# Kernel optimization log

Hardware: AMD Instinct MI355X
Metric: run time of the kernel (lower is better)

Reference implementation:

```python
import jax, jax.numpy as jnp
import numpy as np

N, INC, MID, K = 65536, 256, 64, 16
EPS = 1e-5  # BatchNorm1d default eps


def _bn(x, g, b, m, v):
    # eval-mode BatchNorm1d applied per-channel along the last dim
    return (x - m) * (g * jax.lax.rsqrt(v + EPS)) + b


def setup_inputs() -> dict:
    key = jax.random.key(0)
    ks = jax.random.split(key, 40)
    rn = lambda i, shape, s=0.05: (jax.random.normal(ks[i], shape, jnp.float32) * s)
    pv = lambda i, n: jax.random.uniform(ks[i], (n,), jnp.float32, 0.5, 1.5)  # positive running var
    return {
        "feats": jax.random.normal(ks[0], (N, INC), jnp.float32),
        "pos": jax.random.uniform(ks[1], (N, 3), jnp.float32) * 10.0,
        "idx": jax.random.randint(ks[2], (N, K), 0, N),
        "w_in": rn(3, (MID, INC)),
        "w_q": rn(4, (MID, MID)), "b_q": rn(5, (MID,)),
        "w_k": rn(6, (MID, MID)), "b_k": rn(7, (MID,)),
        "w_v": rn(8, (MID, MID)), "b_v": rn(9, (MID,)),
        # pos_enc: Linear(3,3) -> BN(3) -> ReLU -> Linear(3,mid) -> BN(mid) -> ReLU
        "pe_w1": rn(10, (3, 3)), "pe_b1": rn(11, (3,)),
        "pe_g1": jnp.ones(3), "pe_be1": rn(12, (3,)), "pe_m1": rn(13, (3,)), "pe_v1": pv(14, 3),
        "pe_w2": rn(15, (MID, 3)), "pe_b2": rn(16, (MID,)),
        "pe_g2": jnp.ones(MID), "pe_be2": rn(17, (MID,)), "pe_m2": rn(18, (MID,)), "pe_v2": pv(19, MID),
        # mlp_gamma: Linear(mid,mid) -> BN(mid) -> ReLU -> Linear(mid,mid) -> BN(mid) -> ReLU
        "ga_w1": rn(20, (MID, MID)), "ga_b1": rn(21, (MID,)),
        "ga_g1": jnp.ones(MID), "ga_be1": rn(22, (MID,)), "ga_m1": rn(23, (MID,)), "ga_v1": pv(24, MID),
        "ga_w2": rn(25, (MID, MID)), "ga_b2": rn(26, (MID,)),
        "ga_g2": jnp.ones(MID), "ga_be2": rn(27, (MID,)), "ga_m2": rn(28, (MID,)), "ga_v2": pv(29, MID),
        "w_out": rn(30, (INC, MID)),
    }


def reference(feats, pos, w_in, w_q, b_q, w_k, b_k, w_v, b_v,
              pe_w1, pe_b1, pe_g1, pe_be1, pe_m1, pe_v1,
              pe_w2, pe_b2, pe_g2, pe_be2, pe_m2, pe_v2,
              ga_w1, ga_b1, ga_g1, ga_be1, ga_m1, ga_v1,
              ga_w2, ga_b2, ga_g2, ga_be2, ga_m2, ga_v2,
              w_out, idx):
    xx = feats @ w_in.T                              # [N, mid]
    q = xx @ w_q.T + b_q
    k = xx @ w_k.T + b_k
    v = xx @ w_v.T + b_v
    xv = v[idx]                                      # [N, K, mid] gather
    xk = k[idx]                                      # [N, K, mid]
    xpos = pos[idx]                                  # [N, K, 3]
    # pos_enc
    p = jax.nn.relu(_bn(xpos @ pe_w1.T + pe_b1, pe_g1, pe_be1, pe_m1, pe_v1))
    p = jax.nn.relu(_bn(p @ pe_w2.T + pe_b2, pe_g2, pe_be2, pe_m2, pe_v2))  # [N, K, mid]
    # vector attention logits
    w = xk - q[:, None, :] + p                       # [N, K, mid]
    # mlp_gamma
    w = jax.nn.relu(_bn(w @ ga_w1.T + ga_b1, ga_g1, ga_be1, ga_m1, ga_v1))
    w = jax.nn.relu(_bn(w @ ga_w2.T + ga_b2, ga_g2, ga_be2, ga_m2, ga_v2))
    w = jax.nn.softmax(w, axis=1)                    # softmax over neighbors
    out = jnp.sum((xv + p) * w, axis=1)              # [N, mid]
    out = out @ w_out.T                              # [N, inc]
    return out + feats
```

## Files before the change

kernel.cpp:

```cpp
#include <hip/hip_runtime.h>

#define NPTS 65536
#define INC  256
#define MID  64
#define KNB  16
#define WSTR 72

#define WIN_S   0
#define WQ_S    16384
#define WK_S    20480
#define WV_S    24576
#define GA1_S   28672
#define GA2_S   32768
#define WOUT_S  36864
#define NFRAG_ENT 6656

typedef __attribute__((ext_vector_type(8))) short short8;
typedef __attribute__((ext_vector_type(4))) float f32x4;

#define MFMA(a, b, c) __builtin_amdgcn_mfma_f32_16x16x32_bf16((a), (b), (c), 0, 0, 0)
#define WBAR() __builtin_amdgcn_wave_barrier()

__device__ inline float bf2f(unsigned short s) {
    unsigned int u = ((unsigned int)s) << 16;
    return __builtin_bit_cast(float, u);
}
__device__ inline unsigned int pk_bf16(float lo, float hi) {
    unsigned int r;
    asm("v_cvt_pk_bf16_f32 %0, %1, %2" : "=v"(r) : "v"(lo), "v"(hi));
    return r;
}
__device__ inline short f2bf(float f) { return (short)pk_bf16(f, f); }

__device__ inline short8 cvtf8(f32x4 a, f32x4 b) {
    union { unsigned int u[4]; short8 s; } r;
    r.u[0] = pk_bf16(a[0], a[1]); r.u[1] = pk_bf16(a[2], a[3]);
    r.u[2] = pk_bf16(b[0], b[1]); r.u[3] = pk_bf16(b[2], b[3]);
    return r.s;
}
__device__ inline short8 load_cvt8(const float* __restrict__ p) {
    const f32x4* v = (const f32x4*)p;
    return cvtf8(v[0], v[1]);
}
__device__ inline short8 load_cvt8s(const float* __restrict__ p, float scale) {
    const f32x4* v = (const f32x4*)p;
    f32x4 a = v[0], b = v[1];
    #pragma unroll
    for (int i = 0; i < 4; i++) { a[i] *= scale; b[i] *= scale; }
    return cvtf8(a, b);
}

__global__ __launch_bounds__(256) void k_prep(
    const float* __restrict__ w_in, const float* __restrict__ w_q,
    const float* __restrict__ w_k, const float* __restrict__ w_v,
    const float* __restrict__ ga_w1, const float* __restrict__ ga_w2,
    const float* __restrict__ w_out,
    const float* __restrict__ ga_g1, const float* __restrict__ ga_v1,
    const float* __restrict__ ga_g2, const float* __restrict__ ga_v2,
    short* __restrict__ wbuf)
{
    int gid = blockIdx.x * 256 + threadIdx.x;
    if (gid >= NFRAG_ENT) return;
    if (gid < 2048) {
        int e = gid, f = e >> 6, ln = e & 63;
        int nt = f & 3, ks = f >> 2;
        int row = nt * 16 + (ln & 15), col = ks * 32 + (ln >> 4) * 8;
        *(short8*)&wbuf[(size_t)gid * 8] = load_cvt8(w_in + (size_t)row * INC + col);
    } else if (gid < 4608) {
        int seg = (gid - 2048) >> 9;
        int e = (gid - 2048) & 511;
        const float* m = seg == 0 ? w_q : seg == 1 ? w_k : seg == 2 ? w_v
                       : seg == 3 ? ga_w1 : ga_w2;
        int f = e >> 6, ln = e & 63;
        int nt = f & 3, ks = f >> 2;
        int row = nt * 16 + (ln & 15), col = ks * 32 + (ln >> 4) * 8;
        float scale = 1.f;
        if (seg == 3)      scale = ga_g1[row] * rsqrtf(ga_v1[row] + 1e-5f);
        else if (seg == 4) scale = ga_g2[row] * rsqrtf(ga_v2[row] + 1e-5f);
        *(short8*)&wbuf[(size_t)gid * 8] = load_cvt8s(m + (size_t)row * MID + col, scale);
    } else {
        int e = gid - 4608, f = e >> 6, ln = e & 63;
        int nt = f >> 1, ks = f & 1;
        int row = nt * 16 + (ln & 15), col = ks * 32 + (ln >> 4) * 8;
        *(short8*)&wbuf[(size_t)gid * 8] = load_cvt8(w_out + (size_t)row * MID + col);
    }
}

__global__ __launch_bounds__(256) void k_qkv(
    const float* __restrict__ feats, const short* __restrict__ wfrag,
    const float* __restrict__ pos,
    const float* __restrict__ b_q, const float* __restrict__ b_k,
    const float* __restrict__ b_v,
    const float* __restrict__ pe_w1, const float* __restrict__ pe_b1,
    const float* __restrict__ pe_g1, const float* __restrict__ pe_be1,
    const float* __restrict__ pe_m1, const float* __restrict__ pe_v1,
    const float* __restrict__ pe_w2, const float* __restrict__ pe_b2,
    const float* __restrict__ pe_g2, const float* __restrict__ pe_be2,
    const float* __restrict__ pe_m2, const float* __restrict__ pe_v2,
    const float* __restrict__ ga_b1, const float* __restrict__ ga_g1,
    const float* __restrict__ ga_be1, const float* __restrict__ ga_m1,
    const float* __restrict__ ga_v1,
    short* __restrict__ q1f_out, short* __restrict__ k1_out,
    short* __restrict__ vp_out)
{
    __shared__ __align__(16) short XL[4][16 * WSTR];
    __shared__ float PS[4][16 * 4];
    const int tid = threadIdx.x;
    const int wave = tid >> 6, lane = tid & 63;
    const int l15 = lane & 15, quad = lane >> 4;
    const int rb = (blockIdx.x * 4 + wave) * 16;

    if (lane < 16) {
        float s0 = pe_g1[0] * rsqrtf(pe_v1[0] + 1e-5f);
        float s1 = pe_g1[1] * rsqrtf(pe_v1[1] + 1e-5f);
        float sc = pe_g1[2] * rsqrtf(pe_v1[2] + 1e-5f);
        float px = pos[(size_t)(rb + lane) * 3 + 0];
        float py = pos[(size_t)(rb + lane) * 3 + 1];
        float pz = pos[(size_t)(rb + lane) * 3 + 2];
        PS[wave][lane * 4 + 0] =
            fmaxf((px * pe_w1[0] + py * pe_w1[1] + pz * pe_w1[2] + pe_b1[0] - pe_m1[0]) * s0 + pe_be1[0], 0.f);
        PS[wave][lane * 4 + 1] =
            fmaxf((px * pe_w1[3] + py * pe_w1[4] + pz * pe_w1[5] + pe_b1[1] - pe_m1[1]) * s1 + pe_be1[1], 0.f);
        PS[wave][lane * 4 + 2] =
            fmaxf((px * pe_w1[6] + py * pe_w1[7] + pz * pe_w1[8] + pe_b1[2] - pe_m1[2]) * sc + pe_be1[2], 0.f);
    }

    float w2c0[4], w2c1[4], w2c2[4], s2c[4], sh2c[4], bet1[4], bqc[4], bkc[4], bvc[4];
    #pragma unroll
    for (int nt = 0; nt < 4; nt++) {
        int ch = nt * 16 + l15;
        w2c0[nt] = pe_w2[ch * 3 + 0]; w2c1[nt] = pe_w2[ch * 3 + 1]; w2c2[nt] = pe_w2[ch * 3 + 2];
        float s2 = pe_g2[ch] * rsqrtf(pe_v2[ch] + 1e-5f);
        s2c[nt] = s2;
        sh2c[nt] = (pe_b2[ch] - pe_m2[ch]) * s2 + pe_be2[ch];
        float s1 = ga_g1[ch] * rsqrtf(ga_v1[ch] + 1e-5f);
        bet1[nt] = ga_b1[ch] * s1 + ga_be1[ch] - ga_m1[ch] * s1;
        bqc[nt] = b_q[ch]; bkc[nt] = b_k[ch]; bvc[nt] = b_v[ch];
    }

    f32x4 acc[4];
    #pragma unroll
    for (int nt = 0; nt < 4; nt++) acc[nt] = (f32x4){0.f, 0.f, 0.f, 0.f};
    const float* arow = feats + (size_t)(rb + l15) * INC + quad * 8;
    #pragma unroll
    for (int ks = 0; ks < 8; ks++) {
        short8 a = load_cvt8(arow + ks * 32);
        #pragma unroll
        for (int nt = 0; nt < 4; nt++) {
            short8 b = *(const short8*)&wfrag[WIN_S + (size_t)((ks * 4 + nt) * 64 + lane) * 8];
            acc[nt] = MFMA(a, b, acc[nt]);
        }
    }
    #pragma unroll
    for (int nt = 0; nt < 4; nt++) {
        unsigned int p01 = pk_bf16(acc[nt][0], acc[nt][1]);
        unsigned int p23 = pk_bf16(acc[nt][2], acc[nt][3]);
        XL[wave][(quad * 4 + 0) * WSTR + nt * 16 + l15] = (short)p01;
        XL[wave][(quad * 4 + 1) * WSTR + nt * 16 + l15] = (short)(p01 >> 16);
        XL[wave][(quad * 4 + 2) * WSTR + nt * 16 + l15] = (short)p23;
        XL[wave][(quad * 4 + 3) * WSTR + nt * 16 + l15] = (short)(p23 >> 16);
    }
    WBAR();
    short8 a0 = *(const short8*)&XL[wave][l15 * WSTR + quad * 8];
    short8 a1 = *(const short8*)&XL[wave][l15 * WSTR + 32 + quad * 8];
    WBAR();

    float p10[4], p11[4], p12[4];
    #pragma unroll
    for (int r = 0; r < 4; r++) {
        p10[r] = PS[wave][(quad * 4 + r) * 4 + 0];
        p11[r] = PS[wave][(quad * 4 + r) * 4 + 1];
        p12[r] = PS[wave][(quad * 4 + r) * 4 + 2];
    }
    float pe_[4][4];
    #pragma unroll
    for (int nt = 0; nt < 4; nt++)
        #pragma unroll
        for (int r = 0; r < 4; r++)
            pe_[nt][r] = fmaxf((p10[r] * w2c0[nt] + p11[r] * w2c1[nt] + p12[r] * w2c2[nt])
                               * s2c[nt] + sh2c[nt], 0.f);

    #pragma unroll
    for (int nt = 0; nt < 4; nt++) {
        short8 b0 = *(const short8*)&wfrag[WQ_S + (size_t)((nt) * 64 + lane) * 8];
        short8 b1 = *(const short8*)&wfrag[WQ_S + (size_t)((4 + nt) * 64 + lane) * 8];
        f32x4 c = (f32x4){0.f, 0.f, 0.f, 0.f};
        c = MFMA(a0, b0, c); c = MFMA(a1, b1, c);
        unsigned int p01 = pk_bf16(c[0] + bqc[nt], c[1] + bqc[nt]);
        unsigned int p23 = pk_bf16(c[2] + bqc[nt], c[3] + bqc[nt]);
        XL[wave][(quad * 4 + 0) * WSTR + nt * 16 + l15] = (short)p01;
        XL[wave][(quad * 4 + 1) * WSTR + nt * 16 + l15] = (short)(p01 >> 16);
        XL[wave][(quad * 4 + 2) * WSTR + nt * 16 + l15] = (short)p23;
        XL[wave][(quad * 4 + 3) * WSTR + nt * 16 + l15] = (short)(p23 >> 16);
    }
    WBAR();
    short8 aq0 = *(const short8*)&XL[wave][l15 * WSTR + quad * 8];
    short8 aq1 = *(const short8*)&XL[wave][l15 * WSTR + 32 + quad * 8];
    WBAR();
    #pragma unroll
    for (int nt = 0; nt < 4; nt++) {
        short8 b0 = *(const short8*)&wfrag[GA1_S + (size_t)((nt) * 64 + lane) * 8];
        short8 b1 = *(const short8*)&wfrag[GA1_S + (size_t)((4 + nt) * 64 + lane) * 8];
        f32x4 c = (f32x4){0.f, 0.f, 0.f, 0.f};
        c = MFMA(aq0, b0, c); c = MFMA(aq1, b1, c);
        unsigned int p01 = pk_bf16(c[0] - bet1[nt], c[1] - bet1[nt]);
        unsigned int p23 = pk_bf16(c[2] - bet1[nt], c[3] - bet1[nt]);
        q1f_out[(size_t)(rb + quad * 4 + 0) * MID + nt * 16 + l15] = (short)p01;
        q1f_out[(size_t)(rb + quad * 4 + 1) * MID + nt * 16 + l15] = (short)(p01 >> 16);
        q1f_out[(size_t)(rb + quad * 4 + 2) * MID + nt * 16 + l15] = (short)p23;
        q1f_out[(size_t)(rb + quad * 4 + 3) * MID + nt * 16 + l15] = (short)(p23 >> 16);
    }

    WBAR();
    #pragma unroll
    for (int nt = 0; nt < 4; nt++) {
        short8 b0 = *(const short8*)&wfrag[WK_S + (size_t)((nt) * 64 + lane) * 8];
        short8 b1 = *(const short8*)&wfrag[WK_S + (size_t)((4 + nt) * 64 + lane) * 8];
        f32x4 c = (f32x4){0.f, 0.f, 0.f, 0.f};
        c = MFMA(a0, b0, c); c = MFMA(a1, b1, c);
        unsigned int p01 = pk_bf16(c[0] + bkc[nt] + pe_[nt][0], c[1] + bkc[nt] + pe_[nt][1]);
        unsigned int p23 = pk_bf16(c[2] + bkc[nt] + pe_[nt][2], c[3] + bkc[nt] + pe_[nt][3]);
        XL[wave][(quad * 4 + 0) * WSTR + nt * 16 + l15] = (short)p01;
        XL[wave][(quad * 4 + 1) * WSTR + nt * 16 + l15] = (short)(p01 >> 16);
        XL[wave][(quad * 4 + 2) * WSTR + nt * 16 + l15] = (short)p23;
        XL[wave][(quad * 4 + 3) * WSTR + nt * 16 + l15] = (short)(p23 >> 16);
    }
    WBAR();
    short8 ak0 = *(const short8*)&XL[wave][l15 * WSTR + quad * 8];
    short8 ak1 = *(const short8*)&XL[wave][l15 * WSTR + 32 + quad * 8];
    WBAR();
    #pragma unroll
    for (int nt = 0; nt < 4; nt++) {
        short8 b0 = *(const short8*)&wfrag[GA1_S + (size_t)((nt) * 64 + lane) * 8];
        short8 b1 = *(const short8*)&wfrag[GA1_S + (size_t)((4 + nt) * 64 + lane) * 8];
        f32x4 c = (f32x4){0.f, 0.f, 0.f, 0.f};
        c = MFMA(ak0, b0, c); c = MFMA(ak1, b1, c);
        unsigned int p01 = pk_bf16(c[0], c[1]);
        unsigned int p23 = pk_bf16(c[2], c[3]);
        k1_out[(size_t)(rb + quad * 4 + 0) * MID + nt * 16 + l15] = (short)p01;
        k1_out[(size_t)(rb + quad * 4 + 1) * MID + nt * 16 + l15] = (short)(p01 >> 16);
        k1_out[(size_t)(rb + quad * 4 + 2) * MID + nt * 16 + l15] = (short)p23;
        k1_out[(size_t)(rb + quad * 4 + 3) * MID + nt * 16 + l15] = (short)(p23 >> 16);
    }

    #pragma unroll
    for (int nt = 0; nt < 4; nt++) {
        short8 b0 = *(const short8*)&wfrag[WV_S + (size_t)((nt) * 64 + lane) * 8];
        short8 b1 = *(const short8*)&wfrag[WV_S + (size_t)((4 + nt) * 64 + lane) * 8];
        f32x4 c = (f32x4){0.f, 0.f, 0.f, 0.f};
        c = MFMA(a0, b0, c); c = MFMA(a1, b1, c);
        unsigned int p01 = pk_bf16(c[0] + bvc[nt] + pe_[nt][0], c[1] + bvc[nt] + pe_[nt][1]);
        unsigned int p23 = pk_bf16(c[2] + bvc[nt] + pe_[nt][2], c[3] + bvc[nt] + pe_[nt][3]);
        vp_out[(size_t)(rb + quad * 4 + 0) * MID + nt * 16 + l15] = (short)p01;
        vp_out[(size_t)(rb + quad * 4 + 1) * MID + nt * 16 + l15] = (short)(p01 >> 16);
        vp_out[(size_t)(rb + quad * 4 + 2) * MID + nt * 16 + l15] = (short)p23;
        vp_out[(size_t)(rb + quad * 4 + 3) * MID + nt * 16 + l15] = (short)(p23 >> 16);
    }
}

__global__ __launch_bounds__(256) void k_attn(
    const int* __restrict__ idx,
    const unsigned short* __restrict__ q1f, const unsigned short* __restrict__ k1,
    const unsigned short* __restrict__ vp, const short* __restrict__ wfrag,
    const float* __restrict__ ga_b2, const float* __restrict__ ga_g2,
    const float* __restrict__ ga_be2, const float* __restrict__ ga_m2,
    const float* __restrict__ ga_v2,
    const float* __restrict__ feats, float* __restrict__ out)
{
    __shared__ __align__(16) short BW[512 * 8];
    __shared__ __align__(16) short Wb[4][16 * WSTR];
    __shared__ __align__(16) short OM[16 * WSTR];
    __shared__ float B2[64];
    __shared__ int   JI[4][16];

    const int tid = threadIdx.x;
    const int wave = tid >> 6, lane = tid & 63;
    const int l15 = lane & 15, quad = lane >> 4;

    #pragma unroll
    for (int rep = 0; rep < 2; rep++) {
        int e = rep * 256 + tid;
        *(short8*)&BW[(size_t)e * 8] = *(const short8*)&wfrag[GA2_S + (size_t)e * 8];
    }
    if (tid < 64) {
        float s2 = ga_g2[tid] * rsqrtf(ga_v2[tid] + 1e-5f);
        B2[tid] = ga_b2[tid] * s2 + ga_be2[tid] - ga_m2[tid] * s2;
    }
    __syncthreads();

    const int n0 = blockIdx.x * 16 + wave;
    int m_pref = 0;
    if (lane < 16) m_pref = idx[(size_t)n0 * KNB + lane];
    float qf_pref = bf2f(q1f[(size_t)n0 * MID + lane]);

    #pragma unroll 1
    for (int it = 0; it < 4; it++) {
        const int n = n0 + it * 4;
        if (lane < 16) JI[wave][lane] = m_pref;
        const float qv = qf_pref;
        WBAR();

        unsigned short kr[KNB], vr[KNB];
        #pragma unroll
        for (int j = 0; j < KNB; j++) {
            int m = JI[wave][j];
            kr[j] = k1[(size_t)m * MID + lane];
            vr[j] = vp[(size_t)m * MID + lane];
        }

        if (it < 3) {
            if (lane < 16) m_pref = idx[(size_t)(n + 4) * KNB + lane];
            qf_pref = bf2f(q1f[(size_t)(n + 4) * MID + lane]);
        }

        #pragma unroll
        for (int j = 0; j < KNB; j += 2) {
            float h0 = fmaxf(bf2f(kr[j])     - qv, 0.f);
            float h1 = fmaxf(bf2f(kr[j + 1]) - qv, 0.f);
            unsigned int pk = pk_bf16(h0, h1);
            Wb[wave][(j)     * WSTR + lane] = (short)pk;
            Wb[wave][(j + 1) * WSTR + lane] = (short)(pk >> 16);
        }

        short8 c0 = *(const short8*)&Wb[wave][l15 * WSTR + quad * 8];
        short8 c1 = *(const short8*)&Wb[wave][l15 * WSTR + 32 + quad * 8];
        float sm[4][4];
        #pragma unroll
        for (int nt = 0; nt < 4; nt++) {
            short8 b0 = *(const short8*)&BW[(size_t)((nt) * 64 + lane) * 8];
            short8 b1 = *(const short8*)&BW[(size_t)((4 + nt) * 64 + lane) * 8];
            f32x4 c = (f32x4){0.f, 0.f, 0.f, 0.f};
            c = MFMA(c0, b0, c); c = MFMA(c1, b1, c);
            float b2 = B2[nt * 16 + l15];
            #pragma unroll
            for (int r = 0; r < 4; r++)
                sm[nt][r] = fmaxf(c[r] + b2, 0.f);
        }

        #pragma unroll
        for (int nt = 0; nt < 4; nt++) {
            float mx = fmaxf(fmaxf(sm[nt][0], sm[nt][1]), fmaxf(sm[nt][2], sm[nt][3]));
            mx = fmaxf(mx, __shfl_xor(mx, 16));
            mx = fmaxf(mx, __shfl_xor(mx, 32));
            float e0 = __expf(sm[nt][0] - mx), e1 = __expf(sm[nt][1] - mx);
            float e2 = __expf(sm[nt][2] - mx), e3 = __expf(sm[nt][3] - mx);
            float s = e0 + e1 + e2 + e3;
            s += __shfl_xor(s, 16);
            s += __shfl_xor(s, 32);
            float inv = 1.0f / s;
            unsigned int p01 = pk_bf16(e0 * inv, e1 * inv);
            unsigned int p23 = pk_bf16(e2 * inv, e3 * inv);
            Wb[wave][(quad * 4 + 0) * WSTR + nt * 16 + l15] = (short)p01;
            Wb[wave][(quad * 4 + 1) * WSTR + nt * 16 + l15] = (short)(p01 >> 16);
            Wb[wave][(quad * 4 + 2) * WSTR + nt * 16 + l15] = (short)p23;
            Wb[wave][(quad * 4 + 3) * WSTR + nt * 16 + l15] = (short)(p23 >> 16);
        }

        float oacc = 0.f;
        #pragma unroll
        for (int j = 0; j < KNB; j++)
            oacc += bf2f(vr[j]) * bf2f((unsigned short)Wb[wave][j * WSTR + lane]);
        OM[(it * 4 + wave) * WSTR + lane] = f2bf(oacc);
    }

    __syncthreads();
    short8 A0 = *(const short8*)&OM[l15 * WSTR + quad * 8];
    short8 A1 = *(const short8*)&OM[l15 * WSTR + 32 + quad * 8];
    const int rb = blockIdx.x * 16;
    #pragma unroll
    for (int t = 0; t < 4; t++) {
        int nt = wave * 4 + t;
        short8 b0 = *(const short8*)&wfrag[WOUT_S + (size_t)((nt * 2 + 0) * 64 + lane) * 8];
        short8 b1 = *(const short8*)&wfrag[WOUT_S + (size_t)((nt * 2 + 1) * 64 + lane) * 8];
        f32x4 c = (f32x4){0.f, 0.f, 0.f, 0.f};
        c = MFMA(A0, b0, c);
        c = MFMA(A1, b1, c);
        #pragma unroll
        for (int r = 0; r < 4; r++) {
            size_t off = (size_t)(rb + quad * 4 + r) * INC + nt * 16 + l15;
            out[off] = c[r] + feats[off];
        }
    }
}

extern "C" void kernel_launch(void* const* d_in, const int* in_sizes, int n_in,
                              void* d_out, int out_size, void* d_ws, size_t ws_size,
                              hipStream_t stream)
{
    const float* feats = (const float*)d_in[0];
    const float* pos   = (const float*)d_in[1];
    const int*   idx   = (const int*)d_in[2];
    const float* w_in  = (const float*)d_in[3];
    const float* w_q   = (const float*)d_in[4];
    const float* b_q   = (const float*)d_in[5];
    const float* w_k   = (const float*)d_in[6];
    const float* b_k   = (const float*)d_in[7];
    const float* w_v   = (const float*)d_in[8];
    const float* b_v   = (const float*)d_in[9];
    const float* pe_w1 = (const float*)d_in[10];
    const float* pe_b1 = (const float*)d_in[11];
    const float* pe_g1 = (const float*)d_in[12];
    const float* pe_be1= (const float*)d_in[13];
    const float* pe_m1 = (const float*)d_in[14];
    const float* pe_v1 = (const float*)d_in[15];
    const float* pe_w2 = (const float*)d_in[16];
    const float* pe_b2 = (const float*)d_in[17];
    const float* pe_g2 = (const float*)d_in[18];
    const float* pe_be2= (const float*)d_in[19];
    const float* pe_m2 = (const float*)d_in[20];
    const float* pe_v2 = (const float*)d_in[21];
    const float* ga_w1 = (const float*)d_in[22];
    const float* ga_b1 = (const float*)d_in[23];
    const float* ga_g1 = (const float*)d_in[24];
    const float* ga_be1= (const float*)d_in[25];
    const float* ga_m1 = (const float*)d_in[26];
    const float* ga_v1 = (const float*)d_in[27];
    const float* ga_w2 = (const float*)d_in[28];
    const float* ga_b2 = (const float*)d_in[29];
    const float* ga_g2 = (const float*)d_in[30];
    const float* ga_be2= (const float*)d_in[31];
    const float* ga_m2 = (const float*)d_in[32];
    const float* ga_v2 = (const float*)d_in[33];
    const float* w_out = (const float*)d_in[34];

    char* ws = (char*)d_ws;
    short* q1f   = (short*)(ws);
    short* k1    = (short*)(ws + (size_t) 8 * 1024 * 1024);
    short* vp    = (short*)(ws + (size_t)16 * 1024 * 1024);
    short* wbuf  = (short*)(ws + (size_t)24 * 1024 * 1024);

    k_prep<<<26, 256, 0, stream>>>(w_in, w_q, w_k, w_v, ga_w1, ga_w2, w_out,
                                   ga_g1, ga_v1, ga_g2, ga_v2, wbuf);
    k_qkv<<<NPTS / 64, 256, 0, stream>>>(feats, wbuf, pos, b_q, b_k, b_v,
                                         pe_w1, pe_b1, pe_g1, pe_be1, pe_m1, pe_v1,
                                         pe_w2, pe_b2, pe_g2, pe_be2, pe_m2, pe_v2,
                                         ga_b1, ga_g1, ga_be1, ga_m1, ga_v1,
                                         q1f, k1, vp);
    k_attn<<<NPTS / 16, 256, 0, stream>>>(idx,
                                          (const unsigned short*)q1f,
                                          (const unsigned short*)k1,
                                          (const unsigned short*)vp,
                                          wbuf,
                                          ga_b2, ga_g2, ga_be2, ga_m2, ga_v2,
                                          feats, (float*)d_out);
}
```

Baseline: 258.1 us.

## Interleave K and V into one packed gather buffer and double-buffer neighbor gathers

The qkv kernel now stores k1 and v+pe for each point as one packed 32-bit word, so the attention kernel issues a single 4-byte gather per neighbor and lane instead of two separate 2-byte gathers. The attention loop is unrolled into four explicit stages with two register buffers, so the gather for the next point overlaps the compute of the current one. Neighbor indices for all four points are loaded at once and broadcast with readlane, which removes the shared-memory JI staging and its wave barriers. This costs more registers, since 32 gathered words are live at once, which may lower occupancy.

```diff
diff --git a/kernel.cpp b/kernel.cpp
--- a/kernel.cpp
+++ b/kernel.cpp
@@ -100,8 +100,7 @@
     const float* __restrict__ ga_b1, const float* __restrict__ ga_g1,
     const float* __restrict__ ga_be1, const float* __restrict__ ga_m1,
     const float* __restrict__ ga_v1,
-    short* __restrict__ q1f_out, short* __restrict__ k1_out,
-    short* __restrict__ vp_out)
+    short* __restrict__ q1f_out, unsigned* __restrict__ kv_out)
 {
     __shared__ __align__(16) short XL[4][16 * WSTR];
     __shared__ float PS[4][16 * 4];
@@ -205,10 +204,10 @@
         c = MFMA(aq0, b0, c); c = MFMA(aq1, b1, c);
         unsigned int p01 = pk_bf16(c[0] - bet1[nt], c[1] - bet1[nt]);
         unsigned int p23 = pk_bf16(c[2] - bet1[nt], c[3] - bet1[nt]);
-        q1f_out[(size_t)(rb + quad * 4 + 0) * MID + nt * 16 + l15] = (short)p01;
-        q1f_out[(size_t)(rb + quad * 4 + 1) * MID + nt * 16 + l15] = (short)(p01 >> 16);
-        q1f_out[(size_t)(rb + quad * 4 + 2) * MID + nt * 16 + l15] = (short)p23;
-        q1f_out[(size_t)(rb + quad * 4 + 3) * MID + nt * 16 + l15] = (short)(p23 >> 16);
+        q1f_out[(unsigned)(rb + quad * 4 + 0) * 64u + nt * 16 + l15] = (short)p01;
+        q1f_out[(unsigned)(rb + quad * 4 + 1) * 64u + nt * 16 + l15] = (short)(p01 >> 16);
+        q1f_out[(unsigned)(rb + quad * 4 + 2) * 64u + nt * 16 + l15] = (short)p23;
+        q1f_out[(unsigned)(rb + quad * 4 + 3) * 64u + nt * 16 + l15] = (short)(p23 >> 16);
     }
 
     WBAR();
@@ -229,18 +228,15 @@
     short8 ak0 = *(const short8*)&XL[wave][l15 * WSTR + quad * 8];
     short8 ak1 = *(const short8*)&XL[wave][l15 * WSTR + 32 + quad * 8];
     WBAR();
+    float k1f[4][4];
     #pragma unroll
     for (int nt = 0; nt < 4; nt++) {
         short8 b0 = *(const short8*)&wfrag[GA1_S + (size_t)((nt) * 64 + lane) * 8];
         short8 b1 = *(const short8*)&wfrag[GA1_S + (size_t)((4 + nt) * 64 + lane) * 8];
         f32x4 c = (f32x4){0.f, 0.f, 0.f, 0.f};
         c = MFMA(ak0, b0, c); c = MFMA(ak1, b1, c);
-        unsigned int p01 = pk_bf16(c[0], c[1]);
-        unsigned int p23 = pk_bf16(c[2], c[3]);
-        k1_out[(size_t)(rb + quad * 4 + 0) * MID + nt * 16 + l15] = (short)p01;
-        k1_out[(size_t)(rb + quad * 4 + 1) * MID + nt * 16 + l15] = (short)(p01 >> 16);
-        k1_out[(size_t)(rb + quad * 4 + 2) * MID + nt * 16 + l15] = (short)p23;
-        k1_out[(size_t)(rb + quad * 4 + 3) * MID + nt * 16 + l15] = (short)(p23 >> 16);
+        #pragma unroll
+        for (int r = 0; r < 4; r++) k1f[nt][r] = c[r];
     }
 
     #pragma unroll
@@ -249,19 +245,77 @@
         short8 b1 = *(const short8*)&wfrag[WV_S + (size_t)((4 + nt) * 64 + lane) * 8];
         f32x4 c = (f32x4){0.f, 0.f, 0.f, 0.f};
         c = MFMA(a0, b0, c); c = MFMA(a1, b1, c);
-        unsigned int p01 = pk_bf16(c[0] + bvc[nt] + pe_[nt][0], c[1] + bvc[nt] + pe_[nt][1]);
-        unsigned int p23 = pk_bf16(c[2] + bvc[nt] + pe_[nt][2], c[3] + bvc[nt] + pe_[nt][3]);
-        vp_out[(size_t)(rb + quad * 4 + 0) * MID + nt * 16 + l15] = (short)p01;
-        vp_out[(size_t)(rb + quad * 4 + 1) * MID + nt * 16 + l15] = (short)(p01 >> 16);
-        vp_out[(size_t)(rb + quad * 4 + 2) * MID + nt * 16 + l15] = (short)p23;
-        vp_out[(size_t)(rb + quad * 4 + 3) * MID + nt * 16 + l15] = (short)(p23 >> 16);
-    }
-}
+        #pragma unroll
+        for (int r = 0; r < 4; r++) {
+            float vv = c[r] + bvc[nt] + pe_[nt][r];
+            kv_out[(unsigned)(rb + quad * 4 + r) * 64u + nt * 16 + l15] =
+                pk_bf16(k1f[nt][r], vv);
+        }
+    }
+}
+
+#define GATHER(KVN, IT2)                                                      \
+    _Pragma("unroll")                                                         \
+    for (int j = 0; j < KNB; j++) {                                           \
+        int mj = __builtin_amdgcn_readlane(m_all, (IT2) * 16 + j);            \
+        KVN[j] = kvbuf[(unsigned)mj * 64u + (unsigned)lane];                  \
+    }
+
+#define ATTN_POINT(IT, KV, QV)                                                \
+    {                                                                         \
+        _Pragma("unroll")                                                     \
+        for (int j = 0; j < KNB; j += 2) {                                    \
+            float h0 = fmaxf(__builtin_bit_cast(float, KV[j] << 16) - (QV), 0.f);     \
+            float h1 = fmaxf(__builtin_bit_cast(float, KV[j + 1] << 16) - (QV), 0.f); \
+            unsigned pkw = pk_bf16(h0, h1);                                   \
+            Wb[wave][(j) * WSTR + lane] = (short)pkw;                         \
+            Wb[wave][(j + 1) * WSTR + lane] = (short)(pkw >> 16);             \
+        }                                                                     \
+        short8 c0 = *(const short8*)&Wb[wave][l15 * WSTR + quad * 8];         \
+        short8 c1 = *(const short8*)&Wb[wave][l15 * WSTR + 32 + quad * 8];    \
+        float smv[4][4];                                                      \
+        _Pragma("unroll")                                                     \
+        for (int nt = 0; nt < 4; nt++) {                                      \
+            short8 b0 = *(const short8*)&BW[(size_t)((nt) * 64 + lane) * 8];  \
+            short8 b1 = *(const short8*)&BW[(size_t)((4 + nt) * 64 + lane) * 8]; \
+            f32x4 c = (f32x4){0.f, 0.f, 0.f, 0.f};                            \
+            c = MFMA(c0, b0, c); c = MFMA(c1, b1, c);                         \
+            float b2v = B2[nt * 16 + l15];                                    \
+            _Pragma("unroll")                                                 \
+            for (int r = 0; r < 4; r++)                                       \
+                smv[nt][r] = fmaxf(c[r] + b2v, 0.f);                          \
+        }                                                                     \
+        _Pragma("unroll")                                                     \
+        for (int nt = 0; nt < 4; nt++) {                                      \
+            float mx = fmaxf(fmaxf(smv[nt][0], smv[nt][1]),                   \
+                             fmaxf(smv[nt][2], smv[nt][3]));                  \
+            mx = fmaxf(mx, __shfl_xor(mx, 16));                               \
+            mx = fmaxf(mx, __shfl_xor(mx, 32));                               \
+            float e0 = __expf(smv[nt][0] - mx), e1 = __expf(smv[nt][1] - mx); \
+            float e2 = __expf(smv[nt][2] - mx), e3 = __expf(smv[nt][3] - mx); \
+            float s = e0 + e1 + e2 + e3;                                      \
+            s += __shfl_xor(s, 16);                                           \
+            s += __shfl_xor(s, 32);                                           \
+            float inv = 1.0f / s;                                             \
+            unsigned p01 = pk_bf16(e0 * inv, e1 * inv);                       \
+            unsigned p23 = pk_bf16(e2 * inv, e3 * inv);                       \
+            Wb[wave][(quad * 4 + 0) * WSTR + nt * 16 + l15] = (short)p01;     \
+            Wb[wave][(quad * 4 + 1) * WSTR + nt * 16 + l15] = (short)(p01 >> 16); \
+            Wb[wave][(quad * 4 + 2) * WSTR + nt * 16 + l15] = (short)p23;     \
+            Wb[wave][(quad * 4 + 3) * WSTR + nt * 16 + l15] = (short)(p23 >> 16); \
+        }                                                                     \
+        float oacc = 0.f;                                                     \
+        _Pragma("unroll")                                                     \
+        for (int j = 0; j < KNB; j++)                                         \
+            oacc += __builtin_bit_cast(float, KV[j] & 0xffff0000u)            \
+                    * bf2f((unsigned short)Wb[wave][j * WSTR + lane]);        \
+        OM[((IT) * 4 + wave) * WSTR + lane] = f2bf(oacc);                     \
+    }
 
 __global__ __launch_bounds__(256) void k_attn(
     const int* __restrict__ idx,
-    const unsigned short* __restrict__ q1f, const unsigned short* __restrict__ k1,
-    const unsigned short* __restrict__ vp, const short* __restrict__ wfrag,
+    const unsigned short* __restrict__ q1f,
+    const unsigned* __restrict__ kvbuf, const short* __restrict__ wfrag,
     const float* __restrict__ ga_b2, const float* __restrict__ ga_g2,
     const float* __restrict__ ga_be2, const float* __restrict__ ga_m2,
     const float* __restrict__ ga_v2,
@@ -271,7 +325,6 @@
     __shared__ __align__(16) short Wb[4][16 * WSTR];
     __shared__ __align__(16) short OM[16 * WSTR];
     __shared__ float B2[64];
-    __shared__ int   JI[4][16];
 
     const int tid = threadIdx.x;
     const int wave = tid >> 6, lane = tid & 63;
@@ -289,79 +342,21 @@
     __syncthreads();
 
     const int n0 = blockIdx.x * 16 + wave;
-    int m_pref = 0;
-    if (lane < 16) m_pref = idx[(size_t)n0 * KNB + lane];
-    float qf_pref = bf2f(q1f[(size_t)n0 * MID + lane]);
-
-    #pragma unroll 1
-    for (int it = 0; it < 4; it++) {
-        const int n = n0 + it * 4;
-        if (lane < 16) JI[wave][lane] = m_pref;
-        const float qv = qf_pref;
-        WBAR();
-
-        unsigned short kr[KNB], vr[KNB];
-        #pragma unroll
-        for (int j = 0; j < KNB; j++) {
-            int m = JI[wave][j];
-            kr[j] = k1[(size_t)m * MID + lane];
-            vr[j] = vp[(size_t)m * MID + lane];
-        }
-
-        if (it < 3) {
-            if (lane < 16) m_pref = idx[(size_t)(n + 4) * KNB + lane];
-            qf_pref = bf2f(q1f[(size_t)(n + 4) * MID + lane]);
-        }
-
-        #pragma unroll
-        for (int j = 0; j < KNB; j += 2) {
-            float h0 = fmaxf(bf2f(kr[j])     - qv, 0.f);
-            float h1 = fmaxf(bf2f(kr[j + 1]) - qv, 0.f);
-            unsigned int pk = pk_bf16(h0, h1);
-            Wb[wave][(j)     * WSTR + lane] = (short)pk;
-            Wb[wave][(j + 1) * WSTR + lane] = (short)(pk >> 16);
-        }
-
-        short8 c0 = *(const short8*)&Wb[wave][l15 * WSTR + quad * 8];
-        short8 c1 = *(const short8*)&Wb[wave][l15 * WSTR + 32 + quad * 8];
-        float sm[4][4];
-        #pragma unroll
-        for (int nt = 0; nt < 4; nt++) {
-            short8 b0 = *(const short8*)&BW[(size_t)((nt) * 64 + lane) * 8];
-            short8 b1 = *(const short8*)&BW[(size_t)((4 + nt) * 64 + lane) * 8];
-            f32x4 c = (f32x4){0.f, 0.f, 0.f, 0.f};
-            c = MFMA(c0, b0, c); c = MFMA(c1, b1, c);
-            float b2 = B2[nt * 16 + l15];
-            #pragma unroll
-            for (int r = 0; r < 4; r++)
-                sm[nt][r] = fmaxf(c[r] + b2, 0.f);
-        }
-
-        #pragma unroll
-        for (int nt = 0; nt < 4; nt++) {
-            float mx = fmaxf(fmaxf(sm[nt][0], sm[nt][1]), fmaxf(sm[nt][2], sm[nt][3]));
-            mx = fmaxf(mx, __shfl_xor(mx, 16));
-            mx = fmaxf(mx, __shfl_xor(mx, 32));
-            float e0 = __expf(sm[nt][0] - mx), e1 = __expf(sm[nt][1] - mx);
-            float e2 = __expf(sm[nt][2] - mx), e3 = __expf(sm[nt][3] - mx);
-            float s = e0 + e1 + e2 + e3;
-            s += __shfl_xor(s, 16);
-            s += __shfl_xor(s, 32);
-            float inv = 1.0f / s;
-            unsigned int p01 = pk_bf16(e0 * inv, e1 * inv);
-            unsigned int p23 = pk_bf16(e2 * inv, e3 * inv);
-            Wb[wave][(quad * 4 + 0) * WSTR + nt * 16 + l15] = (short)p01;
-            Wb[wave][(quad * 4 + 1) * WSTR + nt * 16 + l15] = (short)(p01 >> 16);
-            Wb[wave][(quad * 4 + 2) * WSTR + nt * 16 + l15] = (short)p23;
-            Wb[wave][(quad * 4 + 3) * WSTR + nt * 16 + l15] = (short)(p23 >> 16);
-        }
-
-        float oacc = 0.f;
-        #pragma unroll
-        for (int j = 0; j < KNB; j++)
-            oacc += bf2f(vr[j]) * bf2f((unsigned short)Wb[wave][j * WSTR + lane]);
-        OM[(it * 4 + wave) * WSTR + lane] = f2bf(oacc);
-    }
+    int m_all = idx[(unsigned)(n0 + (lane >> 4) * 4) * 16u + (unsigned)(lane & 15)];
+    float qf0 = bf2f(q1f[(unsigned)(n0     ) * 64u + lane]);
+    float qf1 = bf2f(q1f[(unsigned)(n0 +  4) * 64u + lane]);
+    float qf2 = bf2f(q1f[(unsigned)(n0 +  8) * 64u + lane]);
+    float qf3 = bf2f(q1f[(unsigned)(n0 + 12) * 64u + lane]);
+
+    unsigned kvA[KNB], kvB[KNB];
+    GATHER(kvA, 0)
+    GATHER(kvB, 1)
+    ATTN_POINT(0, kvA, qf0)
+    GATHER(kvA, 2)
+    ATTN_POINT(1, kvB, qf1)
+    GATHER(kvB, 3)
+    ATTN_POINT(2, kvA, qf2)
+    ATTN_POINT(3, kvB, qf3)
 
     __syncthreads();
     short8 A0 = *(const short8*)&OM[l15 * WSTR + quad * 8];
@@ -424,10 +419,9 @@
     const float* w_out = (const float*)d_in[34];
 
     char* ws = (char*)d_ws;
-    short* q1f   = (short*)(ws);
-    short* k1    = (short*)(ws + (size_t) 8 * 1024 * 1024);
-    short* vp    = (short*)(ws + (size_t)16 * 1024 * 1024);
-    short* wbuf  = (short*)(ws + (size_t)24 * 1024 * 1024);
+    short*    q1f  = (short*)(ws);
+    unsigned* kv   = (unsigned*)(ws + (size_t) 8 * 1024 * 1024);
+    short*    wbuf = (short*)(ws + (size_t)24 * 1024 * 1024);
 
     k_prep<<<26, 256, 0, stream>>>(w_in, w_q, w_k, w_v, ga_w1, ga_w2, w_out,
                                    ga_g1, ga_v1, ga_g2, ga_v2, wbuf);
@@ -435,12 +429,9 @@
                                          pe_w1, pe_b1, pe_g1, pe_be1, pe_m1, pe_v1,
                                          pe_w2, pe_b2, pe_g2, pe_be2, pe_m2, pe_v2,
                                          ga_b1, ga_g1, ga_be1, ga_m1, ga_v1,
-                                         q1f, k1, vp);
+                                         q1f, kv);
     k_attn<<<NPTS / 16, 256, 0, stream>>>(idx,
-                                          (const unsigned short*)q1f,
-                                          (const unsigned short*)k1,
-                                          (const unsigned short*)vp,
-                                          wbuf,
+                                          (const unsigned short*)q1f, kv, wbuf,
                                           ga_b2, ga_g2, ga_be2, ga_m2, ga_v2,
                                           feats, (float*)d_out);
 }
```

Result: no change. 254.3 us (-1.5%).
